# Performance work log

Hardware: AMD Instinct MI355X
Metric: run time of the kernel (lower is better)

The kernel has to match this reference:

```python
import jax, jax.numpy as jnp
import numpy as np

N_ATOMS = 20
LS_PER_ATOM = [0, 0, 1, 1, 2]   # two s, two p, one d shell per atom
N_PRIM = 8
N_COORDS = 131072


def cart_angulars(l):
    return np.array([[lx, ly, l - lx - ly]
                     for lx in range(l, -1, -1)
                     for ly in range(l - lx, -1, -1)], dtype=np.float32)


def fact2(n):
    n = int(n)
    if n <= 0:
        return 1.0
    r = 1.0
    while n > 1:
        r *= n
        n -= 2
    return r


# ---- static shell bookkeeping (grouped by angular momentum l) ----
SHELL_ATOM = np.array([a for a in range(N_ATOMS) for _ in LS_PER_ATOM])
SHELL_L = np.array([l for _ in range(N_ATOMS) for l in LS_PER_ATOM])
N_SHELLS = len(SHELL_L)
UNIQUE_LS = sorted(set(LS_PER_ATOM))

GROUPS = {}
for l in UNIQUE_LS:
    idx = np.where(SHELL_L == l)[0]
    ls = cart_angulars(l)  # [ncart, 3]
    anorms = 1.0 / np.sqrt(np.array(
        [np.prod([fact2(2 * int(e) - 1) for e in row]) for row in ls],
        dtype=np.float64))
    GROUPS[l] = (idx, ls, anorms.astype(np.float32))

NAO_CART = sum(len(GROUPS[l][1]) * len(GROUPS[l][0]) for l in UNIQUE_LS)  # 280
NAO_SPH = sum((2 * l + 1) * len(GROUPS[l][0]) for l in UNIQUE_LS)          # 260


def setup_inputs() -> dict:
    key = jax.random.key(0)
    k1, k2, k3, k4, k5, k6 = jax.random.split(key, 6)
    coords = jax.random.normal(k1, (N_COORDS, 3), dtype=jnp.float32) * 2.0
    centers = jax.random.normal(k2, (N_ATOMS, 3), dtype=jnp.float32) * 3.0
    # Gaussian exponents must be positive
    zetas = jax.random.uniform(k3, (N_SHELLS, N_PRIM), dtype=jnp.float32,
                               minval=0.2, maxval=3.0)
    coeffs = jax.random.normal(k4, (N_SHELLS, N_PRIM), dtype=jnp.float32)
    normalization = jax.random.uniform(k5, (NAO_CART,), dtype=jnp.float32,
                                       minval=0.5, maxval=1.5)
    cart2sph = jax.random.normal(k6, (NAO_CART, NAO_SPH), dtype=jnp.float32) * 0.3
    return {"coords": coords, "centers": centers, "zetas": zetas,
            "coeffs": coeffs, "normalization": normalization,
            "cart2sph": cart2sph}


def reference(coords, centers, zetas, coeffs, normalization, cart2sph):
    """Batched GTOBasis.eval_ao: [N,3] -> [N, nao_sph]."""
    n = coords.shape[0]
    pieces = []
    for l in UNIQUE_LS:
        idx, ls, anorms = GROUPS[l]
        c = centers[SHELL_ATOM[idx]]                 # [S, 3]
        rs = coords[:, None, :] - c[None]            # [N, S, 3]
        rs2 = jnp.sum(rs * rs, axis=-1)              # [N, S]
        # cartesian angular part: prod over xyz of rs**l_component
        ang = jnp.prod(rs[:, :, None, :] ** jnp.asarray(ls)[None, None],
                       axis=-1)                      # [N, S, ncart]
        ex = jnp.exp(-zetas[idx][None] * rs2[:, :, None])  # [N, S, nprim]
        rad = jnp.sum(coeffs[idx][None] * ex, axis=-1)     # [N, S]
        phis = jnp.asarray(anorms) * ang * rad[:, :, None]  # [N, S, ncart]
        pieces.append(phis.reshape(n, -1))
    aos = jnp.concatenate(pieces, axis=-1) * normalization  # [N, nao_cart]
    return jnp.dot(aos, cart2sph)                           # [N, nao_sph]
```

## Files before the change

### kernel.cpp

```cpp
#include <hip/hip_runtime.h>

typedef unsigned int uint;
typedef unsigned short ushort;
typedef __attribute__((ext_vector_type(8))) short short8;
typedef __attribute__((ext_vector_type(4))) float f32x4;

#define NSH   100
#define NPRIM 8
#define NAOC  280
#define NAOS  260
#define NATOM 20
#define KP    320
#define NKB   10
#define MT    32
#define NTHR  256
#define NCOLP 272
#define BCH   (32 * NCOLP)
#define RSQRT3 0.57735026918962576f
#define LOG2E  1.4426950408889634f
#define EPS   276

#define O_AH    0
#define O_AL    20480
#define O_ZETA  40960
#define O_COEF  44160
#define O_CEN   47360
#define O_CX    47680
#define O_CY    47808
#define O_CZ    47936
#define POOLSZ  48064

__device__ __forceinline__ ushort bf16_rne(float x) {
    uint u = __float_as_uint(x);
    return (ushort)((u + 0x7FFFu + ((u >> 16) & 1u)) >> 16);
}
__device__ __forceinline__ float bf16_to_f(ushort h) {
    return __uint_as_float(((uint)h) << 16);
}
__device__ __forceinline__ uint cvt_pk_bf16(float a, float b) {
    uint r;
    asm("v_cvt_pk_bf16_f32 %0, %1, %2" : "=v"(r) : "v"(a), "v"(b));
    return r;
}

__device__ __forceinline__ float b_src(const float* __restrict__ c2s,
                                       const float* __restrict__ norm,
                                       int kp, int col) {
    if (kp >= KP || col >= NAOS) return 0.0f;
    int a = kp >> 4, i = kp & 15;
    if (i >= 14) return 0.0f;
    int ksrc; float an = 1.0f;
    if (i < 2)      ksrc = 2 * a + i;
    else if (i < 8) ksrc = 40 + 6 * a + (i - 2);
    else {
        ksrc = 160 + 6 * a + (i - 8);
        if (i == 8 || i == 11 || i == 13) an = RSQRT3;
    }
    return c2s[ksrc * NAOS + col] * norm[ksrc] * an;
}

__global__ void prep_b(const float* __restrict__ c2s, const float* __restrict__ norm,
                       ushort* __restrict__ wsHi, ushort* __restrict__ wsLo) {
    int id = blockIdx.x * 256 + threadIdx.x;
    if (id >= KP * NCOLP) return;
    int k = id / NCOLP, col = id % NCOLP;
    float v = b_src(c2s, norm, k, col);
    ushort hi = bf16_rne(v);
    ushort lo = bf16_rne(v - bf16_to_f(hi));
    int off = (k >> 5) * BCH +
              (((col >> 4) * 4 + ((k & 31) >> 3)) * 16 + (col & 15)) * 8 + (k & 7);
    wsHi[off] = hi;
    wsLo[off] = lo;
}

template <bool USEWS>
__global__ __launch_bounds__(NTHR, 3) void gto_mfma(
    const float* __restrict__ coords, const float* __restrict__ centers,
    const float* __restrict__ zetas, const float* __restrict__ coeffs,
    const float* __restrict__ norm, const float* __restrict__ c2s,
    const ushort* __restrict__ wsHi, const ushort* __restrict__ wsLo,
    float* __restrict__ out, int n)
{
    __shared__ __align__(16) char smem[POOLSZ];
    float*  sZeta = (float*)(smem + O_ZETA);
    float*  sCoef = (float*)(smem + O_COEF);
    float4* sCen4 = (float4*)(smem + O_CEN);
    float*  sCx   = (float*)(smem + O_CX);
    float*  sCy   = (float*)(smem + O_CY);
    float*  sCz   = (float*)(smem + O_CZ);

    const int t = threadIdx.x, lane = t & 63, w = t >> 6;
    const int lr = lane & 15, lg4 = lane >> 4;
    const int P0 = blockIdx.x * MT;

    for (int i = t; i < NSH * NPRIM; i += NTHR) {
        sZeta[i] = zetas[i] * LOG2E;
        sCoef[i] = coeffs[i];
    }
    if (t < NATOM)
        sCen4[t] = make_float4(centers[3 * t], centers[3 * t + 1], centers[3 * t + 2], 0.0f);
    if (t < MT * 3) {
        int gi = P0 * 3 + t;
        float v = (gi < 3 * n) ? coords[gi] : 0.0f;
        int p = t / 3, c = t - 3 * (t / 3);
        if (c == 0) sCx[p] = v; else if (c == 1) sCy[p] = v; else sCz[p] = v;
    }
    __syncthreads();

    const int pA = t & 31, ag = t >> 5;
    const float cxp = sCx[pA], cyp = sCy[pA], czp = sCz[pA];

    auto doAtom = [&](int a) {
        float4 ca = sCen4[a];
        float dx = cxp - ca.x, dy = cyp - ca.y, dz = czp - ca.z;
        float r2 = dx * dx + dy * dy + dz * dz;
        float rad[5];
        #pragma unroll
        for (int sh = 0; sh < 5; ++sh) {
            const float* z = &sZeta[(5 * a + sh) * NPRIM];
            const float* cf = &sCoef[(5 * a + sh) * NPRIM];
            float4 z0 = *(const float4*)z,  z1 = *(const float4*)(z + 4);
            float4 c0 = *(const float4*)cf, c1 = *(const float4*)(cf + 4);
            float r = c0.x * __builtin_amdgcn_exp2f(-z0.x * r2);
            r += c0.y * __builtin_amdgcn_exp2f(-z0.y * r2);
            r += c0.z * __builtin_amdgcn_exp2f(-z0.z * r2);
            r += c0.w * __builtin_amdgcn_exp2f(-z0.w * r2);
            r += c1.x * __builtin_amdgcn_exp2f(-z1.x * r2);
            r += c1.y * __builtin_amdgcn_exp2f(-z1.y * r2);
            r += c1.z * __builtin_amdgcn_exp2f(-z1.z * r2);
            r += c1.w * __builtin_amdgcn_exp2f(-z1.w * r2);
            rad[sh] = r;
        }
        float xx = dx * dx, xy = dx * dy, xz = dx * dz;
        float yy = dy * dy, yz = dy * dz, zz = dz * dz;
        float v[14] = { rad[0], rad[1],
                        dx * rad[2], dy * rad[2], dz * rad[2],
                        dx * rad[3], dy * rad[3], dz * rad[3],
                        xx * rad[4], xy * rad[4], xz * rad[4],
                        yy * rad[4], yz * rad[4], zz * rad[4] };
        uint h[7], l[7];
        #pragma unroll
        for (int pr = 0; pr < 7; ++pr) {
            h[pr] = cvt_pk_bf16(v[2 * pr], v[2 * pr + 1]);
            float r0 = v[2 * pr]     - __uint_as_float(h[pr] << 16);
            float r1 = v[2 * pr + 1] - __uint_as_float(h[pr] & 0xffff0000u);
            l[pr] = cvt_pk_bf16(r0, r1);
        }
        const int off = a * 1024 + pA * 16;
        *(uint4*)(smem + O_AH + off)       = make_uint4(h[0], h[1], h[2], h[3]);
        *(uint4*)(smem + O_AH + off + 512) = make_uint4(h[4], h[5], h[6], 0u);
        *(uint4*)(smem + O_AL + off)       = make_uint4(l[0], l[1], l[2], l[3]);
        *(uint4*)(smem + O_AL + off + 512) = make_uint4(l[4], l[5], l[6], 0u);
    };
    if (ag < 4) { doAtom(3 * ag); doAtom(3 * ag + 1); doAtom(3 * ag + 2); }
    else        { int b = 12 + 2 * (ag - 4); doAtom(b); doAtom(b + 1); }
    __syncthreads();

    const ushort* pHb  = wsHi + (4 * w * 64 + lane) * 8;
    const ushort* pLb  = wsLo + (4 * w * 64 + lane) * 8;
    const ushort* pH2b = wsHi + (16 * 64 + lane) * 8;
    const ushort* pL2b = wsLo + (16 * 64 + lane) * 8;

    f32x4 acc[5][2];
    #pragma unroll
    for (int i = 0; i < 5; ++i)
        #pragma unroll
        for (int mt = 0; mt < 2; ++mt)
            acc[i][mt] = (f32x4){0.0f, 0.0f, 0.0f, 0.0f};

    auto loadB = [&](short8 (&bh)[5], short8 (&bl)[5], int kb) {
        const size_t o = (size_t)kb * BCH;
        #pragma unroll
        for (int i = 0; i < 4; ++i) {
            bh[i] = *(const short8*)(pHb + o + i * 512);
            bl[i] = *(const short8*)(pLb + o + i * 512);
        }
        if (w == 0) {
            bh[4] = *(const short8*)(pH2b + o);
            bl[4] = *(const short8*)(pL2b + o);
        }
    };
    auto mfmaChunk = [&](int kb, short8 (&bh)[5], short8 (&bl)[5]) {
        short8 aH[2], aL[2];
        #pragma unroll
        for (int mt = 0; mt < 2; ++mt) {
            const int off = (kb * 4 + lg4) * 512 + (mt * 16 + lr) * 16;
            aH[mt] = *(const short8*)(smem + O_AH + off);
            aL[mt] = *(const short8*)(smem + O_AL + off);
        }
        #pragma unroll
        for (int i = 0; i < 5; ++i) {
            if (i < 4 || w == 0) {
                #pragma unroll
                for (int mt = 0; mt < 2; ++mt)
                    acc[i][mt] = __builtin_amdgcn_mfma_f32_16x16x32_bf16(aH[mt], bh[i], acc[i][mt], 0, 0, 0);
                #pragma unroll
                for (int mt = 0; mt < 2; ++mt)
                    acc[i][mt] = __builtin_amdgcn_mfma_f32_16x16x32_bf16(aH[mt], bl[i], acc[i][mt], 0, 0, 0);
                #pragma unroll
                for (int mt = 0; mt < 2; ++mt)
                    acc[i][mt] = __builtin_amdgcn_mfma_f32_16x16x32_bf16(aL[mt], bh[i], acc[i][mt], 0, 0, 0);
            }
        }
    };

    if (USEWS) {
        short8 bh0[5], bl0[5], bh1[5], bl1[5];
        loadB(bh0, bl0, 0);
        #pragma unroll 1
        for (int kb = 0; kb < NKB; kb += 2) {
            loadB(bh1, bl1, kb + 1);
            mfmaChunk(kb, bh0, bl0);
            if (kb + 2 < NKB) loadB(bh0, bl0, kb + 2);
            mfmaChunk(kb + 1, bh1, bl1);
        }
    } else {
        #pragma unroll 1
        for (int kb = 0; kb < NKB; ++kb) {
            short8 bh[5], bl[5];
            #pragma unroll
            for (int i = 0; i < 5; ++i) {
                int nt = (i == 4) ? 16 : (4 * w + i);
                #pragma unroll
                for (int j = 0; j < 8; ++j) {
                    int k = kb * 32 + lg4 * 8 + j;
                    int col = nt * 16 + lr;
                    float v = b_src(c2s, norm, k, col);
                    ushort hi = bf16_rne(v);
                    bh[i][j] = (short)hi;
                    bl[i][j] = (short)bf16_rne(v - bf16_to_f(hi));
                }
            }
            mfmaChunk(kb, bh, bl);
        }
    }

    __syncthreads();
    float* ep = (float*)smem;
    #pragma unroll
    for (int i = 0; i < 5; ++i) {
        if (i < 4 || w == 0) {
            int nt = (i == 4) ? 16 : (4 * w + i);
            int col = nt * 16 + lr;
            #pragma unroll
            for (int mt = 0; mt < 2; ++mt)
                #pragma unroll
                for (int r = 0; r < 4; ++r)
                    ep[(mt * 16 + lg4 * 4 + r) * EPS + col] = acc[i][mt][r];
        }
    }
    __syncthreads();

    #pragma unroll
    for (int j = 0; j < 8; ++j) {
        int row = w + j * 4;
        int P = P0 + row;
        if (P < n)
            *(float4*)&out[(size_t)P * NAOS + lane * 4] = *(const float4*)&ep[row * EPS + lane * 4];
    }
    if (w == 1 && lane < MT) {
        int P = P0 + lane;
        if (P < n)
            *(float4*)&out[(size_t)P * NAOS + 256] = *(const float4*)&ep[lane * EPS + 256];
    }
}

extern "C" void kernel_launch(void* const* d_in, const int* in_sizes, int n_in,
                              void* d_out, int out_size, void* d_ws, size_t ws_size,
                              hipStream_t stream) {
    const float* coords  = (const float*)d_in[0];
    const float* centers = (const float*)d_in[1];
    const float* zetas   = (const float*)d_in[2];
    const float* coeffs  = (const float*)d_in[3];
    const float* norm    = (const float*)d_in[4];
    const float* c2s     = (const float*)d_in[5];
    float* out = (float*)d_out;
    int n = in_sizes[0] / 3;
    int grid = (n + MT - 1) / MT;

    ushort* wsHi = (ushort*)d_ws;
    ushort* wsLo = wsHi + (size_t)KP * NCOLP;
    const size_t WS_NEED = (size_t)2 * KP * NCOLP * sizeof(ushort);

    if (ws_size >= WS_NEED) {
        prep_b<<<(KP * NCOLP + 255) / 256, 256, 0, stream>>>(c2s, norm, wsHi, wsLo);
        gto_mfma<true><<<grid, NTHR, 0, stream>>>(coords, centers, zetas, coeffs, norm, c2s,
                                                  wsHi, wsLo, out, n);
    } else {
        gto_mfma<false><<<grid, NTHR, 0, stream>>>(coords, centers, zetas, coeffs, norm, c2s,
                                                   nullptr, nullptr, out, n);
    }
}
```

Before: 92.50 us.

## Process two 32-point tiles per block, overlapping second tile's GTO eval with MFMA

Each block now handles 64 points as two 32-row tiles. The second tile's exponential and angular evaluation is interleaved into the first tile's MFMA k-loop, so VALU and transcendental work can overlap matrix work. The per-block setup of zetas, coeffs and centers is also amortised over twice as many points. In exchange the B-operand double-buffer prefetch is dropped in favour of a simple per-chunk load, extra registers hold two accumulator sets and the pending A fragments, and the grid is halved, which may lower occupancy and load balance.

Result: faster. 90.20 us (-2.5%).

```diff
diff --git a/kernel.cpp b/kernel.cpp
--- a/kernel.cpp
+++ b/kernel.cpp
@@ -12,7 +12,7 @@
 #define NATOM 20
 #define KP    320
 #define NKB   10
-#define MT    32
+#define MT    64
 #define NTHR  256
 #define NCOLP 272
 #define BCH   (32 * NCOLP)
@@ -26,9 +26,9 @@
 #define O_COEF  44160
 #define O_CEN   47360
 #define O_CX    47680
-#define O_CY    47808
-#define O_CZ    47936
-#define POOLSZ  48064
+#define O_CY    47936
+#define O_CZ    48192
+#define POOLSZ  48448
 
 __device__ __forceinline__ ushort bf16_rne(float x) {
     uint u = __float_as_uint(x);
@@ -92,6 +92,7 @@
     const int t = threadIdx.x, lane = t & 63, w = t >> 6;
     const int lr = lane & 15, lg4 = lane >> 4;
     const int P0 = blockIdx.x * MT;
+    const int s = t >> 5, pA = t & 31;
 
     for (int i = t; i < NSH * NPRIM; i += NTHR) {
         sZeta[i] = zetas[i] * LOG2E;
@@ -107,10 +108,8 @@
     }
     __syncthreads();
 
-    const int pA = t & 31, ag = t >> 5;
-    const float cxp = sCx[pA], cyp = sCy[pA], czp = sCz[pA];
-
-    auto doAtom = [&](int a) {
+    auto atomEval = [&](int a, float cxp, float cyp, float czp,
+                        uint (&h)[7], uint (&l)[7]) {
         float4 ca = sCen4[a];
         float dx = cxp - ca.x, dy = cyp - ca.y, dz = czp - ca.z;
         float r2 = dx * dx + dy * dy + dz * dz;
@@ -138,7 +137,6 @@
                         dx * rad[3], dy * rad[3], dz * rad[3],
                         xx * rad[4], xy * rad[4], xz * rad[4],
                         yy * rad[4], yz * rad[4], zz * rad[4] };
-        uint h[7], l[7];
         #pragma unroll
         for (int pr = 0; pr < 7; ++pr) {
             h[pr] = cvt_pk_bf16(v[2 * pr], v[2 * pr + 1]);
@@ -146,14 +144,28 @@
             float r1 = v[2 * pr + 1] - __uint_as_float(h[pr] & 0xffff0000u);
             l[pr] = cvt_pk_bf16(r0, r1);
         }
+    };
+    auto dumpCell = [&](int a, uint (&h)[7], uint (&l)[7]) {
         const int off = a * 1024 + pA * 16;
         *(uint4*)(smem + O_AH + off)       = make_uint4(h[0], h[1], h[2], h[3]);
         *(uint4*)(smem + O_AH + off + 512) = make_uint4(h[4], h[5], h[6], 0u);
         *(uint4*)(smem + O_AL + off)       = make_uint4(l[0], l[1], l[2], l[3]);
         *(uint4*)(smem + O_AL + off + 512) = make_uint4(l[4], l[5], l[6], 0u);
     };
-    if (ag < 4) { doAtom(3 * ag); doAtom(3 * ag + 1); doAtom(3 * ag + 2); }
-    else        { int b = 12 + 2 * (ag - 4); doAtom(b); doAtom(b + 1); }
+
+    {
+        const float cx0 = sCx[pA], cy0 = sCy[pA], cz0 = sCz[pA];
+        uint th[7], tl[7];
+        if (s < 4) {
+            atomEval(3 * s, cx0, cy0, cz0, th, tl);     dumpCell(3 * s, th, tl);
+            atomEval(3 * s + 1, cx0, cy0, cz0, th, tl); dumpCell(3 * s + 1, th, tl);
+            atomEval(3 * s + 2, cx0, cy0, cz0, th, tl); dumpCell(3 * s + 2, th, tl);
+        } else {
+            int b = 12 + 2 * (s - 4);
+            atomEval(b, cx0, cy0, cz0, th, tl);     dumpCell(b, th, tl);
+            atomEval(b + 1, cx0, cy0, cz0, th, tl); dumpCell(b + 1, th, tl);
+        }
+    }
     __syncthreads();
 
     const ushort* pHb  = wsHi + (4 * w * 64 + lane) * 8;
@@ -161,26 +173,33 @@
     const ushort* pH2b = wsHi + (16 * 64 + lane) * 8;
     const ushort* pL2b = wsLo + (16 * 64 + lane) * 8;
 
-    f32x4 acc[5][2];
-    #pragma unroll
-    for (int i = 0; i < 5; ++i)
-        #pragma unroll
-        for (int mt = 0; mt < 2; ++mt)
-            acc[i][mt] = (f32x4){0.0f, 0.0f, 0.0f, 0.0f};
-
-    auto loadB = [&](short8 (&bh)[5], short8 (&bl)[5], int kb) {
-        const size_t o = (size_t)kb * BCH;
-        #pragma unroll
-        for (int i = 0; i < 4; ++i) {
-            bh[i] = *(const short8*)(pHb + o + i * 512);
-            bl[i] = *(const short8*)(pLb + o + i * 512);
-        }
-        if (w == 0) {
-            bh[4] = *(const short8*)(pH2b + o);
-            bl[4] = *(const short8*)(pL2b + o);
-        }
-    };
-    auto mfmaChunk = [&](int kb, short8 (&bh)[5], short8 (&bl)[5]) {
+    auto chunkStep = [&](int kb, f32x4 (&acc)[5][2]) {
+        short8 bh[5], bl[5];
+        if (USEWS) {
+            const size_t o = (size_t)kb * BCH;
+            #pragma unroll
+            for (int i = 0; i < 4; ++i) {
+                bh[i] = *(const short8*)(pHb + o + i * 512);
+                bl[i] = *(const short8*)(pLb + o + i * 512);
+            }
+            if (w == 0) {
+                bh[4] = *(const short8*)(pH2b + o);
+                bl[4] = *(const short8*)(pL2b + o);
+            }
+        } else {
+            #pragma unroll
+            for (int i = 0; i < 5; ++i) {
+                int nt = (i == 4) ? 16 : (4 * w + i);
+                #pragma unroll
+                for (int j = 0; j < 8; ++j) {
+                    int k = kb * 32 + lg4 * 8 + j;
+                    float v = b_src(c2s, norm, k, nt * 16 + lr);
+                    ushort hi = bf16_rne(v);
+                    bh[i][j] = (short)hi;
+                    bl[i][j] = (short)bf16_rne(v - bf16_to_f(hi));
+                }
+            }
+        }
         short8 aH[2], aL[2];
         #pragma unroll
         for (int mt = 0; mt < 2; ++mt) {
@@ -204,65 +223,72 @@
         }
     };
 
-    if (USEWS) {
-        short8 bh0[5], bl0[5], bh1[5], bl1[5];
-        loadB(bh0, bl0, 0);
-        #pragma unroll 1
-        for (int kb = 0; kb < NKB; kb += 2) {
-            loadB(bh1, bl1, kb + 1);
-            mfmaChunk(kb, bh0, bl0);
-            if (kb + 2 < NKB) loadB(bh0, bl0, kb + 2);
-            mfmaChunk(kb + 1, bh1, bl1);
-        }
-    } else {
-        #pragma unroll 1
-        for (int kb = 0; kb < NKB; ++kb) {
-            short8 bh[5], bl[5];
-            #pragma unroll
-            for (int i = 0; i < 5; ++i) {
+    f32x4 acc0[5][2];
+    #pragma unroll
+    for (int i = 0; i < 5; ++i)
+        #pragma unroll
+        for (int mt = 0; mt < 2; ++mt)
+            acc0[i][mt] = (f32x4){0.0f, 0.0f, 0.0f, 0.0f};
+
+    const float cx1 = sCx[32 + pA], cy1 = sCy[32 + pA], cz1 = sCz[32 + pA];
+    uint h0[7], l0[7], h1[7], l1[7], h2[7], l2[7];
+    const int aBase = (s < 4) ? 2 * s : 8 + 3 * (s - 4);
+
+    #pragma unroll 1
+    for (int kb = 0; kb < NKB; ++kb) {
+        chunkStep(kb, acc0);
+        if (kb == 2) atomEval(aBase, cx1, cy1, cz1, h0, l0);
+        if (kb == 5) atomEval(aBase + 1, cx1, cy1, cz1, h1, l1);
+        if (kb == 8 && s >= 4) atomEval(aBase + 2, cx1, cy1, cz1, h2, l2);
+    }
+
+    __syncthreads();
+    dumpCell(aBase, h0, l0);
+    dumpCell(aBase + 1, h1, l1);
+    if (s >= 4) dumpCell(aBase + 2, h2, l2);
+    __syncthreads();
+
+    f32x4 acc1[5][2];
+    #pragma unroll
+    for (int i = 0; i < 5; ++i)
+        #pragma unroll
+        for (int mt = 0; mt < 2; ++mt)
+            acc1[i][mt] = (f32x4){0.0f, 0.0f, 0.0f, 0.0f};
+    #pragma unroll 1
+    for (int kb = 0; kb < NKB; ++kb)
+        chunkStep(kb, acc1);
+
+    float* ep = (float*)smem;
+    auto epTile = [&](f32x4 (&acc)[5][2], int rowBase) {
+        __syncthreads();
+        #pragma unroll
+        for (int i = 0; i < 5; ++i) {
+            if (i < 4 || w == 0) {
                 int nt = (i == 4) ? 16 : (4 * w + i);
-                #pragma unroll
-                for (int j = 0; j < 8; ++j) {
-                    int k = kb * 32 + lg4 * 8 + j;
-                    int col = nt * 16 + lr;
-                    float v = b_src(c2s, norm, k, col);
-                    ushort hi = bf16_rne(v);
-                    bh[i][j] = (short)hi;
-                    bl[i][j] = (short)bf16_rne(v - bf16_to_f(hi));
-                }
-            }
-            mfmaChunk(kb, bh, bl);
-        }
-    }
-
-    __syncthreads();
-    float* ep = (float*)smem;
-    #pragma unroll
-    for (int i = 0; i < 5; ++i) {
-        if (i < 4 || w == 0) {
-            int nt = (i == 4) ? 16 : (4 * w + i);
-            int col = nt * 16 + lr;
-            #pragma unroll
-            for (int mt = 0; mt < 2; ++mt)
-                #pragma unroll
-                for (int r = 0; r < 4; ++r)
-                    ep[(mt * 16 + lg4 * 4 + r) * EPS + col] = acc[i][mt][r];
-        }
-    }
-    __syncthreads();
-
-    #pragma unroll
-    for (int j = 0; j < 8; ++j) {
-        int row = w + j * 4;
-        int P = P0 + row;
-        if (P < n)
-            *(float4*)&out[(size_t)P * NAOS + lane * 4] = *(const float4*)&ep[row * EPS + lane * 4];
-    }
-    if (w == 1 && lane < MT) {
-        int P = P0 + lane;
-        if (P < n)
-            *(float4*)&out[(size_t)P * NAOS + 256] = *(const float4*)&ep[lane * EPS + 256];
-    }
+                int col = nt * 16 + lr;
+                #pragma unroll
+                for (int mt = 0; mt < 2; ++mt)
+                    #pragma unroll
+                    for (int r = 0; r < 4; ++r)
+                        ep[(mt * 16 + lg4 * 4 + r) * EPS + col] = acc[i][mt][r];
+            }
+        }
+        __syncthreads();
+        #pragma unroll
+        for (int j = 0; j < 8; ++j) {
+            int row = w + j * 4;
+            int P = P0 + rowBase + row;
+            if (P < n)
+                *(float4*)&out[(size_t)P * NAOS + lane * 4] = *(const float4*)&ep[row * EPS + lane * 4];
+        }
+        if (w == 1 && lane < 32) {
+            int P = P0 + rowBase + lane;
+            if (P < n)
+                *(float4*)&out[(size_t)P * NAOS + 256] = *(const float4*)&ep[lane * EPS + 256];
+        }
+    };
+    epTile(acc0, 0);
+    epTile(acc1, 32);
 }
 
 extern "C" void kernel_launch(void* const* d_in, const int* in_sizes, int n_in,
```

## Warp-specialize kernel: producer waves evaluate AOs while MFMA waves consume tiles

Applied to the files above, without the earlier changes.

Each block now handles 512 points in 16 tiles of 32. Half the waves act as producers, evaluating Gaussian AO values for the next tile, while the other half run the bf16 split MFMA GEMM on the current tile, synchronized with block barriers. The output is written straight from the accumulators with scalar stores instead of through an LDS epilogue. The aim is to overlap exp-heavy VALU work with matrix work and to amortize setup per block. The costs are a grid of only 256 blocks at one block per CU, uncoalesced scalar global stores, and the loss of the B double-buffering.

New measurement: 157.9 us. 1.71x slower.

```diff
diff --git a/kernel.cpp b/kernel.cpp
--- a/kernel.cpp
+++ b/kernel.cpp
@@ -12,13 +12,13 @@
 #define NATOM 20
 #define KP    320
 #define NKB   10
-#define MT    32
-#define NTHR  256
+#define NPTS  512
+#define NTILE 16
+#define NTHR  512
 #define NCOLP 272
 #define BCH   (32 * NCOLP)
 #define RSQRT3 0.57735026918962576f
 #define LOG2E  1.4426950408889634f
-#define EPS   276
 
 #define O_AH    0
 #define O_AL    20480
@@ -26,9 +26,9 @@
 #define O_COEF  44160
 #define O_CEN   47360
 #define O_CX    47680
-#define O_CY    47808
-#define O_CZ    47936
-#define POOLSZ  48064
+#define O_CY    49728
+#define O_CZ    51776
+#define POOLSZ  53824
 
 __device__ __forceinline__ ushort bf16_rne(float x) {
     uint u = __float_as_uint(x);
@@ -74,7 +74,7 @@
 }
 
 template <bool USEWS>
-__global__ __launch_bounds__(NTHR, 3) void gto_mfma(
+__global__ __launch_bounds__(NTHR, 1) void gto_mfma(
     const float* __restrict__ coords, const float* __restrict__ centers,
     const float* __restrict__ zetas, const float* __restrict__ coeffs,
     const float* __restrict__ norm, const float* __restrict__ c2s,
@@ -89,9 +89,8 @@
     float*  sCy   = (float*)(smem + O_CY);
     float*  sCz   = (float*)(smem + O_CZ);
 
-    const int t = threadIdx.x, lane = t & 63, w = t >> 6;
-    const int lr = lane & 15, lg4 = lane >> 4;
-    const int P0 = blockIdx.x * MT;
+    const int t = threadIdx.x;
+    const int P0 = blockIdx.x * NPTS;
 
     for (int i = t; i < NSH * NPRIM; i += NTHR) {
         sZeta[i] = zetas[i] * LOG2E;
@@ -99,18 +98,22 @@
     }
     if (t < NATOM)
         sCen4[t] = make_float4(centers[3 * t], centers[3 * t + 1], centers[3 * t + 2], 0.0f);
-    if (t < MT * 3) {
-        int gi = P0 * 3 + t;
+    for (int i = t; i < NPTS * 3; i += NTHR) {
+        int gi = P0 * 3 + i;
         float v = (gi < 3 * n) ? coords[gi] : 0.0f;
-        int p = t / 3, c = t - 3 * (t / 3);
+        int p = i / 3, c = i - 3 * (i / 3);
         if (c == 0) sCx[p] = v; else if (c == 1) sCy[p] = v; else sCz[p] = v;
     }
-    __syncthreads();
-
-    const int pA = t & 31, ag = t >> 5;
-    const float cxp = sCx[pA], cyp = sCy[pA], czp = sCz[pA];
-
-    auto doAtom = [&](int a) {
+
+    const bool isProd = (t >= 256);
+    const int w = t >> 6, lane = t & 63, lr = lane & 15, lg4 = lane >> 4;
+    const int wc = (w < 4) ? w : 0;
+    const int u = t & 255, s = u >> 5, pAp = u & 31;
+    const int nAtoms = (s < 4) ? 3 : 2;
+    const int aBase  = (s < 4) ? 3 * s : 12 + 2 * (s - 4);
+
+    auto atomEval = [&](int a, float cxp, float cyp, float czp,
+                        uint (&h)[7], uint (&l)[7]) {
         float4 ca = sCen4[a];
         float dx = cxp - ca.x, dy = cyp - ca.y, dz = czp - ca.z;
         float r2 = dx * dx + dy * dy + dz * dz;
@@ -138,7 +141,6 @@
                         dx * rad[3], dy * rad[3], dz * rad[3],
                         xx * rad[4], xy * rad[4], xz * rad[4],
                         yy * rad[4], yz * rad[4], zz * rad[4] };
-        uint h[7], l[7];
         #pragma unroll
         for (int pr = 0; pr < 7; ++pr) {
             h[pr] = cvt_pk_bf16(v[2 * pr], v[2 * pr + 1]);
@@ -146,122 +148,121 @@
             float r1 = v[2 * pr + 1] - __uint_as_float(h[pr] & 0xffff0000u);
             l[pr] = cvt_pk_bf16(r0, r1);
         }
-        const int off = a * 1024 + pA * 16;
+    };
+    auto dumpCell = [&](int a, uint (&h)[7], uint (&l)[7]) {
+        const int off = a * 1024 + pAp * 16;
         *(uint4*)(smem + O_AH + off)       = make_uint4(h[0], h[1], h[2], h[3]);
         *(uint4*)(smem + O_AH + off + 512) = make_uint4(h[4], h[5], h[6], 0u);
         *(uint4*)(smem + O_AL + off)       = make_uint4(l[0], l[1], l[2], l[3]);
         *(uint4*)(smem + O_AL + off + 512) = make_uint4(l[4], l[5], l[6], 0u);
     };
-    if (ag < 4) { doAtom(3 * ag); doAtom(3 * ag + 1); doAtom(3 * ag + 2); }
-    else        { int b = 12 + 2 * (ag - 4); doAtom(b); doAtom(b + 1); }
-    __syncthreads();
-
-    const ushort* pHb  = wsHi + (4 * w * 64 + lane) * 8;
-    const ushort* pLb  = wsLo + (4 * w * 64 + lane) * 8;
+
+    uint h0[7] = {0}, l0[7] = {0}, h1[7] = {0}, l1[7] = {0}, h2[7] = {0}, l2[7] = {0};
+    auto evalTile = [&](int tile) {
+        const int pb = tile * 32 + pAp;
+        const float cx = sCx[pb], cy = sCy[pb], cz = sCz[pb];
+        atomEval(aBase, cx, cy, cz, h0, l0);
+        atomEval(aBase + 1, cx, cy, cz, h1, l1);
+        if (nAtoms == 3) atomEval(aBase + 2, cx, cy, cz, h2, l2);
+    };
+    auto dumpTile = [&]() {
+        dumpCell(aBase, h0, l0);
+        dumpCell(aBase + 1, h1, l1);
+        if (nAtoms == 3) dumpCell(aBase + 2, h2, l2);
+    };
+
+    const ushort* pHb  = wsHi + (4 * wc * 64 + lane) * 8;
+    const ushort* pLb  = wsLo + (4 * wc * 64 + lane) * 8;
     const ushort* pH2b = wsHi + (16 * 64 + lane) * 8;
     const ushort* pL2b = wsLo + (16 * 64 + lane) * 8;
 
-    f32x4 acc[5][2];
-    #pragma unroll
-    for (int i = 0; i < 5; ++i)
-        #pragma unroll
-        for (int mt = 0; mt < 2; ++mt)
-            acc[i][mt] = (f32x4){0.0f, 0.0f, 0.0f, 0.0f};
-
-    auto loadB = [&](short8 (&bh)[5], short8 (&bl)[5], int kb) {
-        const size_t o = (size_t)kb * BCH;
-        #pragma unroll
-        for (int i = 0; i < 4; ++i) {
-            bh[i] = *(const short8*)(pHb + o + i * 512);
-            bl[i] = *(const short8*)(pLb + o + i * 512);
-        }
-        if (w == 0) {
-            bh[4] = *(const short8*)(pH2b + o);
-            bl[4] = *(const short8*)(pL2b + o);
-        }
-    };
-    auto mfmaChunk = [&](int kb, short8 (&bh)[5], short8 (&bl)[5]) {
-        short8 aH[2], aL[2];
-        #pragma unroll
-        for (int mt = 0; mt < 2; ++mt) {
-            const int off = (kb * 4 + lg4) * 512 + (mt * 16 + lr) * 16;
-            aH[mt] = *(const short8*)(smem + O_AH + off);
-            aL[mt] = *(const short8*)(smem + O_AL + off);
-        }
-        #pragma unroll
-        for (int i = 0; i < 5; ++i) {
-            if (i < 4 || w == 0) {
+    __syncthreads();
+    if (isProd) { evalTile(0); dumpTile(); }
+    __syncthreads();
+
+    #pragma unroll 1
+    for (int tl = 0; tl < NTILE; ++tl) {
+        if (!isProd) {
+            f32x4 acc[5][2];
+            #pragma unroll
+            for (int i = 0; i < 5; ++i)
                 #pragma unroll
                 for (int mt = 0; mt < 2; ++mt)
-                    acc[i][mt] = __builtin_amdgcn_mfma_f32_16x16x32_bf16(aH[mt], bh[i], acc[i][mt], 0, 0, 0);
+                    acc[i][mt] = (f32x4){0.0f, 0.0f, 0.0f, 0.0f};
+
+            #pragma unroll 1
+            for (int kb = 0; kb < NKB; ++kb) {
+                short8 bh[5], bl[5];
+                if (USEWS) {
+                    const size_t o = (size_t)kb * BCH;
+                    #pragma unroll
+                    for (int i = 0; i < 4; ++i) {
+                        bh[i] = *(const short8*)(pHb + o + i * 512);
+                        bl[i] = *(const short8*)(pLb + o + i * 512);
+                    }
+                    if (w == 0) {
+                        bh[4] = *(const short8*)(pH2b + o);
+                        bl[4] = *(const short8*)(pL2b + o);
+                    }
+                } else {
+                    #pragma unroll
+                    for (int i = 0; i < 5; ++i) {
+                        int nt = (i == 4) ? 16 : (4 * w + i);
+                        #pragma unroll
+                        for (int j = 0; j < 8; ++j) {
+                            int k = kb * 32 + lg4 * 8 + j;
+                            float v = b_src(c2s, norm, k, nt * 16 + lr);
+                            ushort hi = bf16_rne(v);
+                            bh[i][j] = (short)hi;
+                            bl[i][j] = (short)bf16_rne(v - bf16_to_f(hi));
+                        }
+                    }
+                }
+                short8 aH[2], aL[2];
                 #pragma unroll
-                for (int mt = 0; mt < 2; ++mt)
-                    acc[i][mt] = __builtin_amdgcn_mfma_f32_16x16x32_bf16(aH[mt], bl[i], acc[i][mt], 0, 0, 0);
+                for (int mt = 0; mt < 2; ++mt) {
+                    const int off = (kb * 4 + lg4) * 512 + (mt * 16 + lr) * 16;
+                    aH[mt] = *(const short8*)(smem + O_AH + off);
+                    aL[mt] = *(const short8*)(smem + O_AL + off);
+                }
                 #pragma unroll
-                for (int mt = 0; mt < 2; ++mt)
-                    acc[i][mt] = __builtin_amdgcn_mfma_f32_16x16x32_bf16(aL[mt], bh[i], acc[i][mt], 0, 0, 0);
+                for (int i = 0; i < 5; ++i) {
+                    if (i < 4 || w == 0) {
+                        #pragma unroll
+                        for (int mt = 0; mt < 2; ++mt)
+                            acc[i][mt] = __builtin_amdgcn_mfma_f32_16x16x32_bf16(aH[mt], bh[i], acc[i][mt], 0, 0, 0);
+                        #pragma unroll
+                        for (int mt = 0; mt < 2; ++mt)
+                            acc[i][mt] = __builtin_amdgcn_mfma_f32_16x16x32_bf16(aH[mt], bl[i], acc[i][mt], 0, 0, 0);
+                        #pragma unroll
+                        for (int mt = 0; mt < 2; ++mt)
+                            acc[i][mt] = __builtin_amdgcn_mfma_f32_16x16x32_bf16(aL[mt], bh[i], acc[i][mt], 0, 0, 0);
+                    }
+                }
             }
-        }
-    };
-
-    if (USEWS) {
-        short8 bh0[5], bl0[5], bh1[5], bl1[5];
-        loadB(bh0, bl0, 0);
-        #pragma unroll 1
-        for (int kb = 0; kb < NKB; kb += 2) {
-            loadB(bh1, bl1, kb + 1);
-            mfmaChunk(kb, bh0, bl0);
-            if (kb + 2 < NKB) loadB(bh0, bl0, kb + 2);
-            mfmaChunk(kb + 1, bh1, bl1);
-        }
-    } else {
-        #pragma unroll 1
-        for (int kb = 0; kb < NKB; ++kb) {
-            short8 bh[5], bl[5];
             #pragma unroll
             for (int i = 0; i < 5; ++i) {
-                int nt = (i == 4) ? 16 : (4 * w + i);
-                #pragma unroll
-                for (int j = 0; j < 8; ++j) {
-                    int k = kb * 32 + lg4 * 8 + j;
+                if (i < 4 || w == 0) {
+                    int nt = (i == 4) ? 16 : (4 * w + i);
                     int col = nt * 16 + lr;
-                    float v = b_src(c2s, norm, k, col);
-                    ushort hi = bf16_rne(v);
-                    bh[i][j] = (short)hi;
-                    bl[i][j] = (short)bf16_rne(v - bf16_to_f(hi));
+                    if (col < NAOS) {
+                        #pragma unroll
+                        for (int mt = 0; mt < 2; ++mt) {
+                            #pragma unroll
+                            for (int r = 0; r < 4; ++r) {
+                                int P = P0 + tl * 32 + mt * 16 + lg4 * 4 + r;
+                                if (P < n) out[(size_t)P * NAOS + col] = acc[i][mt][r];
+                            }
+                        }
+                    }
                 }
             }
-            mfmaChunk(kb, bh, bl);
+        } else if (tl + 1 < NTILE) {
+            evalTile(tl + 1);
         }
-    }
-
-    __syncthreads();
-    float* ep = (float*)smem;
-    #pragma unroll
-    for (int i = 0; i < 5; ++i) {
-        if (i < 4 || w == 0) {
-            int nt = (i == 4) ? 16 : (4 * w + i);
-            int col = nt * 16 + lr;
-            #pragma unroll
-            for (int mt = 0; mt < 2; ++mt)
-                #pragma unroll
-                for (int r = 0; r < 4; ++r)
-                    ep[(mt * 16 + lg4 * 4 + r) * EPS + col] = acc[i][mt][r];
-        }
-    }
-    __syncthreads();
-
-    #pragma unroll
-    for (int j = 0; j < 8; ++j) {
-        int row = w + j * 4;
-        int P = P0 + row;
-        if (P < n)
-            *(float4*)&out[(size_t)P * NAOS + lane * 4] = *(const float4*)&ep[row * EPS + lane * 4];
-    }
-    if (w == 1 && lane < MT) {
-        int P = P0 + lane;
-        if (P < n)
-            *(float4*)&out[(size_t)P * NAOS + 256] = *(const float4*)&ep[lane * EPS + 256];
+        __syncthreads();
+        if (isProd && tl + 1 < NTILE) dumpTile();
+        __syncthreads();
     }
 }
 
@@ -276,7 +277,7 @@
     const float* c2s     = (const float*)d_in[5];
     float* out = (float*)d_out;
     int n = in_sizes[0] / 3;
-    int grid = (n + MT - 1) / MT;
+    int grid = (n + NPTS - 1) / NPTS;
 
     ushort* wsHi = (ushort*)d_ws;
     ushort* wsLo = wsHi + (size_t)KP * NCOLP;
```
